# Kernel optimization log

Measured on AMD Instinct MI355X. Metric: run time of the kernel, lower is better.

The kernel has to match this reference:

```python
import jax, jax.numpy as jnp
import numpy as np

C = 512
GROUPS = 32
EPS = 1e-6


def setup_inputs() -> dict:
    key = jax.random.key(0)
    ks = jax.random.split(key, 10)
    B, H, W = 4, 64, 64
    s = 1.0 / np.sqrt(C)
    return {
        "x": jax.random.normal(ks[0], (B, C, H, W), dtype=jnp.float32),
        "gn_weight": jnp.ones((C,), jnp.float32),
        "gn_bias": jnp.zeros((C,), jnp.float32),
        "Wq": jax.random.normal(ks[1], (C, C), jnp.float32) * s,
        "bq": jnp.zeros((C,), jnp.float32),
        "Wk": jax.random.normal(ks[2], (C, C), jnp.float32) * s,
        "bk": jnp.zeros((C,), jnp.float32),
        "Wv": jax.random.normal(ks[3], (C, C), jnp.float32) * s,
        "bv": jnp.zeros((C,), jnp.float32),
        "Wo": jax.random.normal(ks[4], (C, C), jnp.float32) * s,
        "bo": jnp.zeros((C,), jnp.float32),
    }


def _group_norm(x, weight, bias):
    B, Ch, H, W = x.shape
    xg = x.reshape(B, GROUPS, Ch // GROUPS, H, W)
    mean = jnp.mean(xg, axis=(2, 3, 4), keepdims=True)
    var = jnp.var(xg, axis=(2, 3, 4), keepdims=True)
    xg = (xg - mean) * jax.lax.rsqrt(var + EPS)
    h = xg.reshape(B, Ch, H, W)
    return h * weight[None, :, None, None] + bias[None, :, None, None]


def reference(x, gn_weight, gn_bias, Wq, bq, Wk, bk, Wv, bv, Wo, bo):
    B, Ch, H, W = x.shape
    h = _group_norm(x, gn_weight, gn_bias)
    # [B, N, C] with N = H*W spatial tokens
    h = h.reshape(B, Ch, H * W).transpose(0, 2, 1)
    q = h @ Wq.T + bq
    k = h @ Wk.T + bk
    v = h @ Wv.T + bv
    scale = 1.0 / jnp.sqrt(jnp.asarray(Ch, x.dtype))
    scores = jnp.einsum("bnc,bmc->bnm", q, k) * scale  # [B, N, N]
    attn = jax.nn.softmax(scores, axis=-1)
    out = jnp.einsum("bnm,bmc->bnc", attn, v)
    out = out @ Wo.T + bo  # Dropout(0.0) is identity
    out = out.transpose(0, 2, 1).reshape(B, Ch, H, W)
    return x + out
```

## Files before the change

### kernel.cpp

```cpp
#include <hip/hip_runtime.h>
#include <hip/hip_bf16.h>

typedef __attribute__((ext_vector_type(8))) short bf16x8;
typedef __attribute__((ext_vector_type(4))) short bf16x4;
typedef __attribute__((ext_vector_type(4))) float f32x4;

__device__ __forceinline__ short f2bf(float f){
  __hip_bfloat16 h = __float2bfloat16(f);
  return __builtin_bit_cast(short, h);
}
__device__ __forceinline__ float bf2f(short s){
  unsigned u = ((unsigned)(unsigned short)s) << 16;
  return __builtin_bit_cast(float, u);
}

__device__ __forceinline__ void gload_lds16(const short* g, char* l){
  __builtin_amdgcn_global_load_lds(
      (const __attribute__((address_space(1))) void*)g,
      (__attribute__((address_space(3))) void*)l, 16, 0, 0);
}

#define SB0() __builtin_amdgcn_sched_barrier(0)

__global__ __launch_bounds__(256) void gn_stats(const float* __restrict__ x,
// ... 29 lines not shown
                                                short* __restrict__ h){
  __shared__ float tile[128][65];
  int b  = blockIdx.y;
  int n0 = blockIdx.x * 64;
  int t  = threadIdx.x;
  const float* xb = x + (long long)b*512*4096;
  for (int cc = 0; cc < 4; cc++){
    int c0 = cc*128;
    #pragma unroll
    for (int r = 0; r < 128; r += 4){
      int c = r + (t >> 6);
      tile[c][t & 63] = xb[(long long)(c0+c)*4096 + n0 + (t & 63)];
    }
    __syncthreads();
    int n = t >> 2, cp = (t & 3)*32;
    short tmp[32];
    #pragma unroll
    for (int j = 0; j < 32; j++){
      int c = c0 + cp + j;
      float mean = stats[(b*32 + (c >> 4))*2];
      float rstd = stats[(b*32 + (c >> 4))*2 + 1];
      float v = (tile[cp+j][n] - mean)*rstd*gw[c] + gb[c];
      tmp[j] = f2bf(v);
    }
    long long ho = ((long long)b*4096 + n0 + n)*512 + c0 + cp;
    #pragma unroll
    for (int j2 = 0; j2 < 4; j2++){
      bf16x8 v8;
      #pragma unroll
      for (int e = 0; e < 8; e++) v8[e] = tmp[j2*8 + e];
      *(bf16x8*)&h[ho + j2*8] = v8;
    }
    __syncthreads();
  }
}

__global__ __launch_bounds__(256) void f2bf_all(
    const float* __restrict__ w0, const float* __restrict__ w1,
    const float* __restrict__ w2, const float* __restrict__ w3,
    short* __restrict__ o0, short* __restrict__ o1,
    short* __restrict__ o2, short* __restrict__ o3){
  int idx = blockIdx.x*256 + threadIdx.x;
  int m = idx >> 15, r = idx & 32767;
  const float* src = (m==0) ? w0 : (m==1) ? w1 : (m==2) ? w2 : w3;
  short* dst       = (m==0) ? o0 : (m==1) ? o1 : (m==2) ? o2 : o3;
  const float4* p = (const float4*)src + (long long)r*2;
  float4 a = p[0], c = p[1];
  bf16x8 v;
  v[0]=f2bf(a.x); v[1]=f2bf(a.y); v[2]=f2bf(a.z); v[3]=f2bf(a.w);
  v[4]=f2bf(c.x); v[5]=f2bf(c.y); v[6]=f2bf(c.z); v[7]=f2bf(c.w);
  *(bf16x8*)&dst[(long long)r*8] = v;
}

__global__ __launch_bounds__(256) void reduce_den(const float* __restrict__ partial,
                                                  float* __restrict__ inv_den,
                                                  int nrows){
  int r = blockIdx.x*256 + threadIdx.x;
  if (r >= nrows) return;
  const float4* p = (const float4*)(partial + (long long)r*16);
  float4 a = p[0], b = p[1], c = p[2], d = p[3];
  float s = a.x+a.y+a.z+a.w + b.x+b.y+b.z+b.w + c.x+c.y+c.z+c.w + d.x+d.y+d.z+d.w;
  inv_den[r] = 1.f / s;
}

template<int MODE, int BN, int SWZ>
__global__ __launch_bounds__(512, 2) void gemmF(
    const short* __restrict__ A, const short* __restrict__ Bw,
    const float* __restrict__ bias,
    void* __restrict__ outp, const float* __restrict__ resid,
    int M, int Nn, int Kd,
    long long sA, long long sB, long long sO, float scale,
    const float* __restrict__ dptr, float* __restrict__ partial)
{
  constexpr int WARPS_N = BN/64;
  constexpr int WARPS_M = 8/WARPS_N;
  constexpr int WM = 256/WARPS_M;
  constexpr int MF = WM/16;
  constexpr int ABYT = 32768;
  constexpr int BBYT = BN*128;
  constexpr int BUFSZ = ABYT + BBYT;
  constexpr int BH = BBYT/16384;
  constexpr int LOADS = 4 + 2*BH;
  extern __shared__ char smem[];

  int bx, by, bz;
  if constexpr (SWZ == 1){
    int id = blockIdx.x;
    int xcd = id & 7, s = id >> 3;
    int region = xcd + ((s >> 4) << 3);
    int o = s & 15;
    bz = region >> 4;
    bx = (region & 3)*4 + (o & 3);
    by = ((region >> 2) & 3)*4 + (o >> 2);
  } else if constexpr (SWZ == 2){
    int id = blockIdx.x;
    int xcd = id & 7, s = id >> 3;
    int combo = xcd*2 + (s & 1);
    by = combo & 3; bz = combo >> 2;
    bx = s >> 1;
  } else { bx = blockIdx.x; by = blockIdx.y; bz = blockIdx.z; }

  const short* Ab = A + bz*sA;
  const short* Bb = Bw + bz*sB;
  const int m0 = bx*256, n0 = by*BN;
  const int t = threadIdx.x;
  const int lane = t & 63, wid = t >> 6;
  const int g = lane >> 4, lr = lane & 15;
  const int wr = wid / WARPS_N, wc = wid % WARPS_N;
  const long long KdLL = Kd;

  const int r0 = t >> 3, c8 = t & 7;

  auto STAGE_A = [&](int kt, int buf, int h){
    char* d = smem + buf*BUFSZ + h*16384 + t*16;
    #pragma unroll
    for (int j = 0; j < 2; j++){
      int row = h*128 + j*64 + r0;
      gload_lds16(Ab + (long long)(m0+row)*KdLL + (long long)kt*64 + ((c8 ^ (row&7))*8),
                  d + j*8192);
    }
  };
  auto STAGE_B = [&](int kt, int buf, int h){
    char* d = smem + buf*BUFSZ + ABYT + h*16384 + t*16;
    #pragma unroll
    for (int j = 0; j < 2; j++){
      int row = h*128 + j*64 + r0;
      gload_lds16(Bb + (long long)(n0+row)*KdLL + (long long)kt*64 + ((c8 ^ (row&7))*8),
                  d + j*8192);
    }
  };

  int roA[MF], swA[MF], roB[4], swB[4];
  #pragma unroll
  for (int mf = 0; mf < MF; mf++){
    int ra = wr*WM + mf*16 + lr;
    roA[mf] = (ra>>7)*16384 + (ra&127)*128; swA[mf] = ra & 7;
  }
  #pragma unroll
  for (int nf = 0; nf < 4; nf++){
    int rb = wc*64 + nf*16 + lr;
    roB[nf] = ABYT + (rb>>7)*16384 + (rb&127)*128; swB[nf] = rb & 7;
  }

  f32x4 acc[MF][4];
  #pragma unroll
  for (int i = 0; i < MF; i++)
    #pragma unroll
    for (int j = 0; j < 4; j++)
      acc[i][j] = f32x4{0.f,0.f,0.f,0.f};

  const int NT = Kd >> 6;

  STAGE_A(0,0,0); STAGE_A(0,0,1);
  STAGE_B(0,0,0); if constexpr (BH==2) STAGE_B(0,0,1);
  STAGE_A(1,1,0); STAGE_A(1,1,1);
  STAGE_B(1,1,0); if constexpr (BH==2) STAGE_B(1,1,1);
  if constexpr (BH==2) asm volatile("s_waitcnt vmcnt(8)":::"memory");
  else                 asm volatile("s_waitcnt vmcnt(6)":::"memory");
  SB0();
  __builtin_amdgcn_s_barrier();

  for (int kt = 0; kt < NT; ++kt){
    char* base = smem + (kt & 1)*BUFSZ;
    bf16x8 av[MF][2], bv[4][2];
    #pragma unroll
    for (int n = 0; n < 4; n++)
      #pragma unroll
      for (int ks = 0; ks < 2; ks++)
        bv[n][ks] = *(const bf16x8*)(base + roB[n] + (((ks*4+g) ^ swB[n])<<4));
    #pragma unroll
    for (int m = 0; m < MF; m++)
      #pragma unroll
      for (int ks = 0; ks < 2; ks++)
        av[m][ks] = *(const bf16x8*)(base + roA[m] + (((ks*4+g) ^ swA[m])<<4));
    #pragma unroll
    for (int ks = 0; ks < 2; ks++)
      #pragma unroll
      for (int m = 0; m < MF; m++)
        #pragma unroll
        for (int n = 0; n < 4; n++){
          if constexpr (MODE == 1 || MODE == 2)
            acc[m][n] = __builtin_amdgcn_mfma_f32_16x16x32_bf16(av[m][ks], bv[n][ks], acc[m][n], 0,0,0);
          else
            acc[m][n] = __builtin_amdgcn_mfma_f32_16x16x32_bf16(bv[n][ks], av[m][ks], acc[m][n], 0,0,0);
        }
    SB0();
    __builtin_amdgcn_s_barrier();
    SB0();
    if (kt + 2 < NT){
      STAGE_A(kt+2, kt&1, 0); STAGE_A(kt+2, kt&1, 1);
      STAGE_B(kt+2, kt&1, 0); if constexpr (BH==2) STAGE_B(kt+2, kt&1, 1);
      if constexpr (BH==2) asm volatile("s_waitcnt vmcnt(8)":::"memory");
      else                 asm volatile("s_waitcnt vmcnt(6)":::"memory");
    } else {
      asm volatile("s_waitcnt vmcnt(0)":::"memory");
    }
    __builtin_amdgcn_s_barrier();
  }

  if constexpr (MODE == 0){
    short* outb = (short*)outp + bz*sO;
    const bool hb = (bias != nullptr);
    #pragma unroll
    for (int mi = 0; mi < MF; mi++){
      int row = m0 + wr*WM + mi*16 + lr;
      #pragma unroll
      for (int ni = 0; ni < 4; ni++){
        int col = n0 + wc*64 + ni*16 + g*4;
        float b0=0.f,b1=0.f,b2=0.f,b3=0.f;
        if (hb){ float4 bb = *(const float4*)&bias[col]; b0=bb.x; b1=bb.y; b2=bb.z; b3=bb.w; }
        bf16x4 pk;
        pk[0] = f2bf((acc[mi][ni][0] + b0)*scale);
        pk[1] = f2bf((acc[mi][ni][1] + b1)*scale);
        pk[2] = f2bf((acc[mi][ni][2] + b2)*scale);
        pk[3] = f2bf((acc[mi][ni][3] + b3)*scale);
        *(bf16x4*)&outb[(long long)row*Nn + col] = pk;
      }
    }
  } else if constexpr (MODE == 4){
    short* outb = (short*)outp + bz*sO;
    float* rowpart = (float*)smem;
    constexpr float LOG2E = 1.4426950408889634f;
    #pragma unroll
    for (int mi = 0; mi < MF; mi++){
      int lrow = wr*WM + mi*16 + lr;
      int row  = m0 + lrow;
      float rs = 0.f;
      #pragma unroll
      for (int ni = 0; ni < 4; ni++){
        int col = n0 + wc*64 + ni*16 + g*4;
        bf16x4 pk;
        #pragma unroll
        for (int i = 0; i < 4; i++){
          float p = exp2f(acc[mi][ni][i]*LOG2E);
          rs += p;
          pk[i] = f2bf(p);
        }
        *(bf16x4*)&outb[(long long)row*Nn + col] = pk;
      }
      rs += __shfl_xor(rs, 16);
      rs += __shfl_xor(rs, 32);
      if (g == 0) rowpart[lrow*WARPS_N + wc] = rs;
    }
    __syncthreads();
    if (t < 256){
      float s2 = 0.f;
      #pragma unroll
      for (int j = 0; j < WARPS_N; j++) s2 += rowpart[t*WARPS_N + j];
      partial[((long long)bz*4096 + m0 + t)*16 + by] = s2;
    }
  } else if constexpr (MODE == 5){
    short* outb = (short*)outp + bz*sO;
    const float* dd = dptr + (long long)bz*M;
    #pragma unroll
    for (int mi = 0; mi < MF; mi++){
      int row = m0 + wr*WM + mi*16 + lr;
      float inv = dd[row];
      #pragma unroll
      for (int ni = 0; ni < 4; ni++){
        int col = n0 + wc*64 + ni*16 + g*4;
        bf16x4 pk;
        #pragma unroll
        for (int i = 0; i < 4; i++) pk[i] = f2bf(acc[mi][ni][i]*inv);
        *(bf16x4*)&outb[(long long)row*Nn + col] = pk;
      }
    }
  } else if constexpr (MODE == 1){
    short* outb = (short*)outp + bz*sO;
    #pragma unroll
    for (int ni = 0; ni < 4; ni++){
      int col = n0 + wc*64 + ni*16 + lr;
      float bv2 = bias ? bias[col] : 0.f;
      #pragma unroll
      for (int mi = 0; mi < MF; mi++){
        int row = m0 + wr*WM + mi*16 + g*4;
        bf16x4 pk;
        #pragma unroll
        for (int i = 0; i < 4; i++) pk[i] = f2bf((acc[mi][ni][i] + bv2)*scale);
        *(bf16x4*)&outb[(long long)col*M + row] = pk;
      }
    }
  } else {
    float* outb = (float*)outp + bz*sO;
    const float* rx = resid + bz*sO;
    #pragma unroll
    for (int ni = 0; ni < 4; ni++){
      int col = n0 + wc*64 + ni*16 + lr;
      float bv2 = bias[col];
      #pragma unroll
      for (int mi = 0; mi < MF; mi++){
        int row = m0 + wr*WM + mi*16 + g*4;
        long long off = (long long)col*M + row;
        float4 xr = *(const float4*)&rx[off];
        float4 o;
        o.x = acc[mi][ni][0] + bv2 + xr.x;
        o.y = acc[mi][ni][1] + bv2 + xr.y;
        o.z = acc[mi][ni][2] + bv2 + xr.z;
        o.w = acc[mi][ni][3] + bv2 + xr.w;
        *(float4*)&outb[off] = o;
      }
    }
  }
}

extern "C" void kernel_launch(void* const* d_in, const int* in_sizes, int n_in,
                              void* d_out, int out_size, void* d_ws, size_t ws_size,
                              hipStream_t stream)
{
  const float* x   = (const float*)d_in[0];
  const float* gnw = (const float*)d_in[1];
  const float* gnb = (const float*)d_in[2];
  const float* Wq  = (const float*)d_in[3];
  const float* bq  = (const float*)d_in[4];
  const float* Wk  = (const float*)d_in[5];
  const float* bk  = (const float*)d_in[6];
  const float* Wv  = (const float*)d_in[7];
  const float* bvp = (const float*)d_in[8];
  const float* Wo  = (const float*)d_in[9];
  const float* bo  = (const float*)d_in[10];
  float* out = (float*)d_out;

  char* ws = (char*)d_ws;
  const size_t MB = 1ull << 20;
  short* h      = (short*)(ws);
  short* q      = (short*)(ws + 16*MB);
  short* kmat   = (short*)(ws + 32*MB);
  short* vt     = (short*)(ws + 48*MB);
  short* ao     = (short*)(ws + 64*MB);
  short* wqb    = (short*)(ws + 80*MB);
  short* wkb    = wqb + 262144;
  short* wvb    = wkb + 262144;
  short* wob    = wvb + 262144;
  float* stats  = (float*)(ws + 82*MB);
  float* inv_den= (float*)(ws + 82*MB + 8192);
  float* partial= (float*)(ws + 83*MB);
  short* S      = (short*)(ws + 84*MB);

  const int LDS256 = 131072, LDS128 = 98304;
  hipFuncSetAttribute(reinterpret_cast<const void*>(&gemmF<4,256,1>),
                      hipFuncAttributeMaxDynamicSharedMemorySize, LDS256);
  hipFuncSetAttribute(reinterpret_cast<const void*>(&gemmF<4,256,0>),
                      hipFuncAttributeMaxDynamicSharedMemorySize, LDS256);
  hipFuncSetAttribute(reinterpret_cast<const void*>(&gemmF<0,128,0>),
                      hipFuncAttributeMaxDynamicSharedMemorySize, LDS128);
  hipFuncSetAttribute(reinterpret_cast<const void*>(&gemmF<1,128,0>),
                      hipFuncAttributeMaxDynamicSharedMemorySize, LDS128);
  hipFuncSetAttribute(reinterpret_cast<const void*>(&gemmF<2,128,0>),
                      hipFuncAttributeMaxDynamicSharedMemorySize, LDS128);
  hipFuncSetAttribute(reinterpret_cast<const void*>(&gemmF<5,128,2>),
                      hipFuncAttributeMaxDynamicSharedMemorySize, LDS128);
  hipFuncSetAttribute(reinterpret_cast<const void*>(&gemmF<5,128,0>),
                      hipFuncAttributeMaxDynamicSharedMemorySize, LDS128);

  dim3 blk(256);
  dim3 blk512(512);
  gn_stats<<<dim3(128), blk, 0, stream>>>(x, stats);
  gn_apply<<<dim3(64,4), blk, 0, stream>>>(x, stats, gnw, gnb, h);
  f2bf_all<<<dim3(512), blk, 0, stream>>>(Wq, Wk, Wv, Wo, wqb, wkb, wvb, wob);

  const long long sTok = 4096ll*512;
  const long long sS   = 4096ll*4096;
  const float qscale = 0.044194173824159216f;

  gemmF<0,128,0><<<dim3(16,4,4), blk512, LDS128, stream>>>(h, wqb, bq,  q,    nullptr, 4096, 512, 512, sTok, 0, sTok, qscale, nullptr, nullptr);
  gemmF<0,128,0><<<dim3(16,4,4), blk512, LDS128, stream>>>(h, wkb, bk,  kmat, nullptr, 4096, 512, 512, sTok, 0, sTok, 1.f, nullptr, nullptr);
  gemmF<1,128,0><<<dim3(16,4,4), blk512, LDS128, stream>>>(h, wvb, bvp, vt,   nullptr, 4096, 512, 512, sTok, 0, sTok, 1.f, nullptr, nullptr);

  if (ws_size >= 212*MB){
    gemmF<4,256,1><<<dim3(1024), blk512, LDS256, stream>>>(q, kmat, nullptr, S, nullptr, 4096, 4096, 512, sTok, sTok, sS, 1.f, nullptr, partial);
    reduce_den<<<dim3(64), blk, 0, stream>>>(partial, inv_den, 16384);
    gemmF<5,128,2><<<dim3(256), blk512, LDS128, stream>>>(S, vt, nullptr, ao, nullptr, 4096, 512, 4096, sS, sTok, sTok, 1.f, inv_den, nullptr);
  } else {
    for (int b = 0; b < 4; b++){
      gemmF<4,256,0><<<dim3(16,16,1), blk512, LDS256, stream>>>(q + b*sTok, kmat + b*sTok, nullptr, S, nullptr, 4096, 4096, 512, 0, 0, 0, 1.f, nullptr, partial);
      reduce_den<<<dim3(16), blk, 0, stream>>>(partial, inv_den, 4096);
      gemmF<5,128,0><<<dim3(16,4,1), blk512, LDS128, stream>>>(S, vt + b*sTok, nullptr, ao + b*sTok, nullptr, 4096, 512, 4096, 0, 0, 0, 1.f, inv_den, nullptr);
    }
  }

  gemmF<2,128,0><<<dim3(16,4,4), blk512, LDS128, stream>>>(ao, wob, bo, out, x, 4096, 512, 512, sTok, 0, sTok, 1.f, nullptr, nullptr);
}
```

Before: 317.0 us.

## Rework GEMM to 256-thread blocks with K=32 stages and fewer warps

```diff
diff --git a/kernel.cpp b/kernel.cpp
--- a/kernel.cpp
+++ b/kernel.cpp
@@ -117,7 +117,7 @@
 }
 
 template<int MODE, int BN, int SWZ>
-__global__ __launch_bounds__(512, 2) void gemmF(
+__global__ __launch_bounds__(256, 1) void gemmW(
     const short* __restrict__ A, const short* __restrict__ Bw,
     const float* __restrict__ bias,
     void* __restrict__ outp, const float* __restrict__ resid,
@@ -125,15 +125,13 @@
     long long sA, long long sB, long long sO, float scale,
     const float* __restrict__ dptr, float* __restrict__ partial)
 {
-  constexpr int WARPS_N = BN/64;
-  constexpr int WARPS_M = 8/WARPS_N;
-  constexpr int WM = 256/WARPS_M;
-  constexpr int MF = WM/16;
-  constexpr int ABYT = 32768;
-  constexpr int BBYT = BN*128;
+  constexpr int WN = BN/2;
+  constexpr int MF = 8;
+  constexpr int NF = WN/16;
+  constexpr int ABYT = 16384;
+  constexpr int BBYT = BN*64;
   constexpr int BUFSZ = ABYT + BBYT;
-  constexpr int BH = BBYT/16384;
-  constexpr int LOADS = 4 + 2*BH;
+  constexpr int NBG = BN/64;
   extern __shared__ char smem[];
 
   int bx, by, bz;
@@ -159,92 +157,82 @@
   const int t = threadIdx.x;
   const int lane = t & 63, wid = t >> 6;
   const int g = lane >> 4, lr = lane & 15;
-  const int wr = wid / WARPS_N, wc = wid % WARPS_N;
+  const int wr = wid >> 1, wc = wid & 1;
   const long long KdLL = Kd;
 
-  const int r0 = t >> 3, c8 = t & 7;
-
-  auto STAGE_A = [&](int kt, int buf, int h){
-    char* d = smem + buf*BUFSZ + h*16384 + t*16;
-    #pragma unroll
-    for (int j = 0; j < 2; j++){
-      int row = h*128 + j*64 + r0;
-      gload_lds16(Ab + (long long)(m0+row)*KdLL + (long long)kt*64 + ((c8 ^ (row&7))*8),
-                  d + j*8192);
-    }
+  const int srow = t >> 2;
+  const int sch  = (t & 3) ^ ((t >> 3) & 3);
+  const short* pA[4]; const short* pB[NBG];
+  #pragma unroll
+  for (int j = 0; j < 4; j++)
+    pA[j] = Ab + (long long)(m0 + j*64 + srow)*KdLL + sch*8;
+  #pragma unroll
+  for (int j = 0; j < NBG; j++)
+    pB[j] = Bb + (long long)(n0 + j*64 + srow)*KdLL + sch*8;
+  const int t16 = t*16;
+
+  int offA[MF], offB[NF];
+  #pragma unroll
+  for (int mf = 0; mf < MF; mf++){
+    int ra = wr*128 + mf*16 + lr;
+    offA[mf] = ra*64 + ((g ^ ((ra >> 1) & 3)) << 4);
+  }
+  #pragma unroll
+  for (int nf = 0; nf < NF; nf++){
+    int rb = wc*WN + nf*16 + lr;
+    offB[nf] = ABYT + rb*64 + ((g ^ ((rb >> 1) & 3)) << 4);
+  }
+
+  f32x4 acc[MF][NF];
+  #pragma unroll
+  for (int i = 0; i < MF; i++)
+    #pragma unroll
+    for (int j = 0; j < NF; j++)
+      acc[i][j] = f32x4{0.f,0.f,0.f,0.f};
+
+  auto STAGE = [&](int kt, int buf){
+    char* d = smem + buf*BUFSZ;
+    const long long ko = (long long)kt*32;
+    #pragma unroll
+    for (int j = 0; j < 4; j++)
+      gload_lds16(pA[j] + ko, d + j*4096 + t16);
+    #pragma unroll
+    for (int j = 0; j < NBG; j++)
+      gload_lds16(pB[j] + ko, d + ABYT + j*4096 + t16);
   };
-  auto STAGE_B = [&](int kt, int buf, int h){
-    char* d = smem + buf*BUFSZ + ABYT + h*16384 + t*16;
-    #pragma unroll
-    for (int j = 0; j < 2; j++){
-      int row = h*128 + j*64 + r0;
-      gload_lds16(Bb + (long long)(n0+row)*KdLL + (long long)kt*64 + ((c8 ^ (row&7))*8),
-                  d + j*8192);
-    }
-  };
-
-  int roA[MF], swA[MF], roB[4], swB[4];
-  #pragma unroll
-  for (int mf = 0; mf < MF; mf++){
-    int ra = wr*WM + mf*16 + lr;
-    roA[mf] = (ra>>7)*16384 + (ra&127)*128; swA[mf] = ra & 7;
-  }
-  #pragma unroll
-  for (int nf = 0; nf < 4; nf++){
-    int rb = wc*64 + nf*16 + lr;
-    roB[nf] = ABYT + (rb>>7)*16384 + (rb&127)*128; swB[nf] = rb & 7;
-  }
-
-  f32x4 acc[MF][4];
-  #pragma unroll
-  for (int i = 0; i < MF; i++)
-    #pragma unroll
-    for (int j = 0; j < 4; j++)
-      acc[i][j] = f32x4{0.f,0.f,0.f,0.f};
-
-  const int NT = Kd >> 6;
-
-  STAGE_A(0,0,0); STAGE_A(0,0,1);
-  STAGE_B(0,0,0); if constexpr (BH==2) STAGE_B(0,0,1);
-  STAGE_A(1,1,0); STAGE_A(1,1,1);
-  STAGE_B(1,1,0); if constexpr (BH==2) STAGE_B(1,1,1);
-  if constexpr (BH==2) asm volatile("s_waitcnt vmcnt(8)":::"memory");
-  else                 asm volatile("s_waitcnt vmcnt(6)":::"memory");
+
+  const int NT = Kd >> 5;
+
+  STAGE(0, 0);
+  STAGE(1, 1);
+  if constexpr (NBG == 4) asm volatile("s_waitcnt vmcnt(8)":::"memory");
+  else                    asm volatile("s_waitcnt vmcnt(6)":::"memory");
   SB0();
   __builtin_amdgcn_s_barrier();
 
   for (int kt = 0; kt < NT; ++kt){
     char* base = smem + (kt & 1)*BUFSZ;
-    bf16x8 av[MF][2], bv[4][2];
-    #pragma unroll
-    for (int n = 0; n < 4; n++)
-      #pragma unroll
-      for (int ks = 0; ks < 2; ks++)
-        bv[n][ks] = *(const bf16x8*)(base + roB[n] + (((ks*4+g) ^ swB[n])<<4));
+    bf16x8 av[MF], bv[NF];
+    #pragma unroll
+    for (int n = 0; n < NF; n++) bv[n] = *(const bf16x8*)(base + offB[n]);
+    #pragma unroll
+    for (int m = 0; m < MF; m++) av[m] = *(const bf16x8*)(base + offA[m]);
     #pragma unroll
     for (int m = 0; m < MF; m++)
       #pragma unroll
-      for (int ks = 0; ks < 2; ks++)
-        av[m][ks] = *(const bf16x8*)(base + roA[m] + (((ks*4+g) ^ swA[m])<<4));
-    #pragma unroll
-    for (int ks = 0; ks < 2; ks++)
-      #pragma unroll
-      for (int m = 0; m < MF; m++)
-        #pragma unroll
-        for (int n = 0; n < 4; n++){
-          if constexpr (MODE == 1 || MODE == 2)
-            acc[m][n] = __builtin_amdgcn_mfma_f32_16x16x32_bf16(av[m][ks], bv[n][ks], acc[m][n], 0,0,0);
-          else
-            acc[m][n] = __builtin_amdgcn_mfma_f32_16x16x32_bf16(bv[n][ks], av[m][ks], acc[m][n], 0,0,0);
-        }
+      for (int n = 0; n < NF; n++){
+        if constexpr (MODE == 1 || MODE == 2)
+          acc[m][n] = __builtin_amdgcn_mfma_f32_16x16x32_bf16(av[m], bv[n], acc[m][n], 0,0,0);
+        else
+          acc[m][n] = __builtin_amdgcn_mfma_f32_16x16x32_bf16(bv[n], av[m], acc[m][n], 0,0,0);
+      }
     SB0();
     __builtin_amdgcn_s_barrier();
     SB0();
     if (kt + 2 < NT){
-      STAGE_A(kt+2, kt&1, 0); STAGE_A(kt+2, kt&1, 1);
-      STAGE_B(kt+2, kt&1, 0); if constexpr (BH==2) STAGE_B(kt+2, kt&1, 1);
-      if constexpr (BH==2) asm volatile("s_waitcnt vmcnt(8)":::"memory");
-      else                 asm volatile("s_waitcnt vmcnt(6)":::"memory");
+      STAGE(kt + 2, kt & 1);
+      if constexpr (NBG == 4) asm volatile("s_waitcnt vmcnt(8)":::"memory");
+      else                    asm volatile("s_waitcnt vmcnt(6)":::"memory");
     } else {
       asm volatile("s_waitcnt vmcnt(0)":::"memory");
     }
@@ -256,10 +244,10 @@
     const bool hb = (bias != nullptr);
     #pragma unroll
     for (int mi = 0; mi < MF; mi++){
-      int row = m0 + wr*WM + mi*16 + lr;
-      #pragma unroll
-      for (int ni = 0; ni < 4; ni++){
-        int col = n0 + wc*64 + ni*16 + g*4;
+      int row = m0 + wr*128 + mi*16 + lr;
+      #pragma unroll
+      for (int ni = 0; ni < NF; ni++){
+        int col = n0 + wc*WN + ni*16 + g*4;
         float b0=0.f,b1=0.f,b2=0.f,b3=0.f;
         if (hb){ float4 bb = *(const float4*)&bias[col]; b0=bb.x; b1=bb.y; b2=bb.z; b3=bb.w; }
         bf16x4 pk;
@@ -276,12 +264,12 @@
     constexpr float LOG2E = 1.4426950408889634f;
     #pragma unroll
     for (int mi = 0; mi < MF; mi++){
-      int lrow = wr*WM + mi*16 + lr;
+      int lrow = wr*128 + mi*16 + lr;
       int row  = m0 + lrow;
       float rs = 0.f;
       #pragma unroll
-      for (int ni = 0; ni < 4; ni++){
-        int col = n0 + wc*64 + ni*16 + g*4;
+      for (int ni = 0; ni < NF; ni++){
+        int col = n0 + wc*WN + ni*16 + g*4;
         bf16x4 pk;
         #pragma unroll
         for (int i = 0; i < 4; i++){
@@ -293,13 +281,11 @@
       }
       rs += __shfl_xor(rs, 16);
       rs += __shfl_xor(rs, 32);
-      if (g == 0) rowpart[lrow*WARPS_N + wc] = rs;
+      if (g == 0) rowpart[lrow*2 + wc] = rs;
     }
     __syncthreads();
-    if (t < 256){
-      float s2 = 0.f;
-      #pragma unroll
-      for (int j = 0; j < WARPS_N; j++) s2 += rowpart[t*WARPS_N + j];
+    {
+      float s2 = rowpart[t*2] + rowpart[t*2 + 1];
       partial[((long long)bz*4096 + m0 + t)*16 + by] = s2;
     }
   } else if constexpr (MODE == 5){
@@ -307,11 +293,11 @@
     const float* dd = dptr + (long long)bz*M;
     #pragma unroll
     for (int mi = 0; mi < MF; mi++){
-      int row = m0 + wr*WM + mi*16 + lr;
+      int row = m0 + wr*128 + mi*16 + lr;
       float inv = dd[row];
       #pragma unroll
-      for (int ni = 0; ni < 4; ni++){
-        int col = n0 + wc*64 + ni*16 + g*4;
+      for (int ni = 0; ni < NF; ni++){
+        int col = n0 + wc*WN + ni*16 + g*4;
         bf16x4 pk;
         #pragma unroll
         for (int i = 0; i < 4; i++) pk[i] = f2bf(acc[mi][ni][i]*inv);
@@ -321,12 +307,12 @@
   } else if constexpr (MODE == 1){
     short* outb = (short*)outp + bz*sO;
     #pragma unroll
-    for (int ni = 0; ni < 4; ni++){
-      int col = n0 + wc*64 + ni*16 + lr;
+    for (int ni = 0; ni < NF; ni++){
+      int col = n0 + wc*WN + ni*16 + lr;
       float bv2 = bias ? bias[col] : 0.f;
       #pragma unroll
       for (int mi = 0; mi < MF; mi++){
-        int row = m0 + wr*WM + mi*16 + g*4;
+        int row = m0 + wr*128 + mi*16 + g*4;
         bf16x4 pk;
         #pragma unroll
         for (int i = 0; i < 4; i++) pk[i] = f2bf((acc[mi][ni][i] + bv2)*scale);
@@ -337,12 +323,12 @@
     float* outb = (float*)outp + bz*sO;
     const float* rx = resid + bz*sO;
     #pragma unroll
-    for (int ni = 0; ni < 4; ni++){
-      int col = n0 + wc*64 + ni*16 + lr;
+    for (int ni = 0; ni < NF; ni++){
+      int col = n0 + wc*WN + ni*16 + lr;
       float bv2 = bias[col];
       #pragma unroll
       for (int mi = 0; mi < MF; mi++){
-        int row = m0 + wr*WM + mi*16 + g*4;
+        int row = m0 + wr*128 + mi*16 + g*4;
         long long off = (long long)col*M + row;
         float4 xr = *(const float4*)&rx[off];
         float4 o;
@@ -389,24 +375,9 @@
   float* partial= (float*)(ws + 83*MB);
   short* S      = (short*)(ws + 84*MB);
 
-  const int LDS256 = 131072, LDS128 = 98304;
-  hipFuncSetAttribute(reinterpret_cast<const void*>(&gemmF<4,256,1>),
-                      hipFuncAttributeMaxDynamicSharedMemorySize, LDS256);
-  hipFuncSetAttribute(reinterpret_cast<const void*>(&gemmF<4,256,0>),
-                      hipFuncAttributeMaxDynamicSharedMemorySize, LDS256);
-  hipFuncSetAttribute(reinterpret_cast<const void*>(&gemmF<0,128,0>),
-                      hipFuncAttributeMaxDynamicSharedMemorySize, LDS128);
-  hipFuncSetAttribute(reinterpret_cast<const void*>(&gemmF<1,128,0>),
-                      hipFuncAttributeMaxDynamicSharedMemorySize, LDS128);
-  hipFuncSetAttribute(reinterpret_cast<const void*>(&gemmF<2,128,0>),
-                      hipFuncAttributeMaxDynamicSharedMemorySize, LDS128);
-  hipFuncSetAttribute(reinterpret_cast<const void*>(&gemmF<5,128,2>),
-                      hipFuncAttributeMaxDynamicSharedMemorySize, LDS128);
-  hipFuncSetAttribute(reinterpret_cast<const void*>(&gemmF<5,128,0>),
-                      hipFuncAttributeMaxDynamicSharedMemorySize, LDS128);
+  const int SH256 = 65536, SH128 = 49152;
 
   dim3 blk(256);
-  dim3 blk512(512);
   gn_stats<<<dim3(128), blk, 0, stream>>>(x, stats);
   gn_apply<<<dim3(64,4), blk, 0, stream>>>(x, stats, gnw, gnb, h);
   f2bf_all<<<dim3(512), blk, 0, stream>>>(Wq, Wk, Wv, Wo, wqb, wkb, wvb, wob);
@@ -415,21 +386,21 @@
   const long long sS   = 4096ll*4096;
   const float qscale = 0.044194173824159216f;
 
-  gemmF<0,128,0><<<dim3(16,4,4), blk512, LDS128, stream>>>(h, wqb, bq,  q,    nullptr, 4096, 512, 512, sTok, 0, sTok, qscale, nullptr, nullptr);
-  gemmF<0,128,0><<<dim3(16,4,4), blk512, LDS128, stream>>>(h, wkb, bk,  kmat, nullptr, 4096, 512, 512, sTok, 0, sTok, 1.f, nullptr, nullptr);
-  gemmF<1,128,0><<<dim3(16,4,4), blk512, LDS128, stream>>>(h, wvb, bvp, vt,   nullptr, 4096, 512, 512, sTok, 0, sTok, 1.f, nullptr, nullptr);
+  gemmW<0,128,0><<<dim3(16,4,4), blk, SH128, stream>>>(h, wqb, bq,  q,    nullptr, 4096, 512, 512, sTok, 0, sTok, qscale, nullptr, nullptr);
+  gemmW<0,128,0><<<dim3(16,4,4), blk, SH128, stream>>>(h, wkb, bk,  kmat, nullptr, 4096, 512, 512, sTok, 0, sTok, 1.f, nullptr, nullptr);
+  gemmW<1,128,0><<<dim3(16,4,4), blk, SH128, stream>>>(h, wvb, bvp, vt,   nullptr, 4096, 512, 512, sTok, 0, sTok, 1.f, nullptr, nullptr);
 
   if (ws_size >= 212*MB){
-    gemmF<4,256,1><<<dim3(1024), blk512, LDS256, stream>>>(q, kmat, nullptr, S, nullptr, 4096, 4096, 512, sTok, sTok, sS, 1.f, nullptr, partial);
+    gemmW<4,256,1><<<dim3(1024), blk, SH256, stream>>>(q, kmat, nullptr, S, nullptr, 4096, 4096, 512, sTok, sTok, sS, 1.f, nullptr, partial);
     reduce_den<<<dim3(64), blk, 0, stream>>>(partial, inv_den, 16384);
-    gemmF<5,128,2><<<dim3(256), blk512, LDS128, stream>>>(S, vt, nullptr, ao, nullptr, 4096, 512, 4096, sS, sTok, sTok, 1.f, inv_den, nullptr);
+    gemmW<5,128,2><<<dim3(256), blk, SH128, stream>>>(S, vt, nullptr, ao, nullptr, 4096, 512, 4096, sS, sTok, sTok, 1.f, inv_den, nullptr);
   } else {
     for (int b = 0; b < 4; b++){
-      gemmF<4,256,0><<<dim3(16,16,1), blk512, LDS256, stream>>>(q + b*sTok, kmat + b*sTok, nullptr, S, nullptr, 4096, 4096, 512, 0, 0, 0, 1.f, nullptr, partial);
+      gemmW<4,256,0><<<dim3(16,16,1), blk, SH256, stream>>>(q + b*sTok, kmat + b*sTok, nullptr, S, nullptr, 4096, 4096, 512, 0, 0, 0, 1.f, nullptr, partial);
       reduce_den<<<dim3(16), blk, 0, stream>>>(partial, inv_den, 4096);
-      gemmF<5,128,0><<<dim3(16,4,1), blk512, LDS128, stream>>>(S, vt + b*sTok, nullptr, ao + b*sTok, nullptr, 4096, 512, 4096, 0, 0, 0, 1.f, inv_den, nullptr);
-    }
-  }
-
-  gemmF<2,128,0><<<dim3(16,4,4), blk512, LDS128, stream>>>(ao, wob, bo, out, x, 4096, 512, 512, sTok, 0, sTok, 1.f, nullptr, nullptr);
-}
+      gemmW<5,128,0><<<dim3(16,4,1), blk, SH128, stream>>>(S, vt + b*sTok, nullptr, ao + b*sTok, nullptr, 4096, 512, 4096, 0, 0, 0, 1.f, inv_den, nullptr);
+    }
+  }
+
+  gemmW<2,128,0><<<dim3(16,4,4), blk, SH128, stream>>>(ao, wob, bo, out, x, 4096, 512, 512, sTok, 0, sTok, 1.f, nullptr, nullptr);
+}
```

Measured after the change: 396.3 us. 25.0% more time.

## Load GEMM B-operand directly from global into registers, stage only A in LDS

Applied to the files above, without the earlier changes.

```diff
diff --git a/kernel.cpp b/kernel.cpp
--- a/kernel.cpp
+++ b/kernel.cpp
@@ -117,7 +117,7 @@
 }
 
 template<int MODE, int BN, int SWZ>
-__global__ __launch_bounds__(512, 2) void gemmF(
+__global__ __launch_bounds__(512, 2) void gemmG(
     const short* __restrict__ A, const short* __restrict__ Bw,
     const float* __restrict__ bias,
     void* __restrict__ outp, const float* __restrict__ resid,
@@ -126,14 +126,11 @@
     const float* __restrict__ dptr, float* __restrict__ partial)
 {
   constexpr int WARPS_N = BN/64;
-  constexpr int WARPS_M = 8/WARPS_N;
-  constexpr int WM = 256/WARPS_M;
+  constexpr int WM = 256/(8/WARPS_N);
   constexpr int MF = WM/16;
+  constexpr int MH = (MF > 4) ? 2 : 1;
+  constexpr int MFH = MF/MH;
   constexpr int ABYT = 32768;
-  constexpr int BBYT = BN*128;
-  constexpr int BUFSZ = ABYT + BBYT;
-  constexpr int BH = BBYT/16384;
-  constexpr int LOADS = 4 + 2*BH;
   extern __shared__ char smem[];
 
   int bx, by, bz;
@@ -165,7 +162,7 @@
   const int r0 = t >> 3, c8 = t & 7;
 
   auto STAGE_A = [&](int kt, int buf, int h){
-    char* d = smem + buf*BUFSZ + h*16384 + t*16;
+    char* d = smem + buf*ABYT + h*16384 + t*16;
     #pragma unroll
     for (int j = 0; j < 2; j++){
       int row = h*128 + j*64 + r0;
@@ -173,27 +170,24 @@
                   d + j*8192);
     }
   };
-  auto STAGE_B = [&](int kt, int buf, int h){
-    char* d = smem + buf*BUFSZ + ABYT + h*16384 + t*16;
-    #pragma unroll
-    for (int j = 0; j < 2; j++){
-      int row = h*128 + j*64 + r0;
-      gload_lds16(Bb + (long long)(n0+row)*KdLL + (long long)kt*64 + ((c8 ^ (row&7))*8),
-                  d + j*8192);
-    }
-  };
-
-  int roA[MF], swA[MF], roB[4], swB[4];
+
+  int roA[MF], swA[MF];
   #pragma unroll
   for (int mf = 0; mf < MF; mf++){
     int ra = wr*WM + mf*16 + lr;
     roA[mf] = (ra>>7)*16384 + (ra&127)*128; swA[mf] = ra & 7;
   }
-  #pragma unroll
-  for (int nf = 0; nf < 4; nf++){
-    int rb = wc*64 + nf*16 + lr;
-    roB[nf] = ABYT + (rb>>7)*16384 + (rb&127)*128; swB[nf] = rb & 7;
-  }
+
+  const short* pBf = Bb + (long long)(n0 + wc*64 + lr)*KdLL + g*8;
+
+  #define LOAD_BV(DST, KT) do{                                            \
+    _Pragma("unroll")                                                     \
+    for (int _n = 0; _n < 4; _n++)                                        \
+      _Pragma("unroll")                                                   \
+      for (int _ks = 0; _ks < 2; _ks++)                                   \
+        DST[_n][_ks] = *(const bf16x8*)(pBf + (long long)_n*16*KdLL +     \
+                         (long long)(KT)*64 + _ks*32);                    \
+  }while(0)
 
   f32x4 acc[MF][4];
   #pragma unroll
@@ -202,53 +196,51 @@
     for (int j = 0; j < 4; j++)
       acc[i][j] = f32x4{0.f,0.f,0.f,0.f};
 
+  bf16x8 bvA[4][2], bvB[4][2];
   const int NT = Kd >> 6;
 
   STAGE_A(0,0,0); STAGE_A(0,0,1);
-  STAGE_B(0,0,0); if constexpr (BH==2) STAGE_B(0,0,1);
   STAGE_A(1,1,0); STAGE_A(1,1,1);
-  STAGE_B(1,1,0); if constexpr (BH==2) STAGE_B(1,1,1);
-  if constexpr (BH==2) asm volatile("s_waitcnt vmcnt(8)":::"memory");
-  else                 asm volatile("s_waitcnt vmcnt(6)":::"memory");
+  LOAD_BV(bvA, 0);
+  asm volatile("s_waitcnt vmcnt(0)":::"memory");
   SB0();
   __builtin_amdgcn_s_barrier();
 
-  for (int kt = 0; kt < NT; ++kt){
-    char* base = smem + (kt & 1)*BUFSZ;
-    bf16x8 av[MF][2], bv[4][2];
-    #pragma unroll
-    for (int n = 0; n < 4; n++)
-      #pragma unroll
-      for (int ks = 0; ks < 2; ks++)
-        bv[n][ks] = *(const bf16x8*)(base + roB[n] + (((ks*4+g) ^ swB[n])<<4));
-    #pragma unroll
-    for (int m = 0; m < MF; m++)
-      #pragma unroll
-      for (int ks = 0; ks < 2; ks++)
-        av[m][ks] = *(const bf16x8*)(base + roA[m] + (((ks*4+g) ^ swA[m])<<4));
-    #pragma unroll
-    for (int ks = 0; ks < 2; ks++)
-      #pragma unroll
-      for (int m = 0; m < MF; m++)
+  auto BODY = [&](int kt, bf16x8 (&bvC)[4][2], bf16x8 (&bvN)[4][2]){
+    char* base = smem + (kt & 1)*ABYT;
+    if (kt + 1 < NT) LOAD_BV(bvN, kt + 1);
+    #pragma unroll
+    for (int h = 0; h < MH; h++){
+      bf16x8 av[MFH][2];
+      #pragma unroll
+      for (int m = 0; m < MFH; m++)
         #pragma unroll
-        for (int n = 0; n < 4; n++){
-          if constexpr (MODE == 1 || MODE == 2)
-            acc[m][n] = __builtin_amdgcn_mfma_f32_16x16x32_bf16(av[m][ks], bv[n][ks], acc[m][n], 0,0,0);
-          else
-            acc[m][n] = __builtin_amdgcn_mfma_f32_16x16x32_bf16(bv[n][ks], av[m][ks], acc[m][n], 0,0,0);
-        }
+        for (int ks = 0; ks < 2; ks++)
+          av[m][ks] = *(const bf16x8*)(base + roA[h*MFH+m] +
+                        (((ks*4+g) ^ swA[h*MFH+m])<<4));
+      #pragma unroll
+      for (int m = 0; m < MFH; m++)
+        #pragma unroll
+        for (int n = 0; n < 4; n++)
+          #pragma unroll
+          for (int ks = 0; ks < 2; ks++){
+            if constexpr (MODE == 1 || MODE == 2)
+              acc[h*MFH+m][n] = __builtin_amdgcn_mfma_f32_16x16x32_bf16(av[m][ks], bvC[n][ks], acc[h*MFH+m][n], 0,0,0);
+            else
+              acc[h*MFH+m][n] = __builtin_amdgcn_mfma_f32_16x16x32_bf16(bvC[n][ks], av[m][ks], acc[h*MFH+m][n], 0,0,0);
+          }
+    }
     SB0();
     __builtin_amdgcn_s_barrier();
     SB0();
-    if (kt + 2 < NT){
-      STAGE_A(kt+2, kt&1, 0); STAGE_A(kt+2, kt&1, 1);
-      STAGE_B(kt+2, kt&1, 0); if constexpr (BH==2) STAGE_B(kt+2, kt&1, 1);
-      if constexpr (BH==2) asm volatile("s_waitcnt vmcnt(8)":::"memory");
-      else                 asm volatile("s_waitcnt vmcnt(6)":::"memory");
-    } else {
-      asm volatile("s_waitcnt vmcnt(0)":::"memory");
-    }
+    if (kt + 2 < NT){ STAGE_A(kt+2, kt&1, 0); STAGE_A(kt+2, kt&1, 1); }
+    asm volatile("s_waitcnt vmcnt(0)":::"memory");
     __builtin_amdgcn_s_barrier();
+  };
+
+  for (int kt = 0; kt < NT; kt += 2){
+    BODY(kt,     bvA, bvB);
+    BODY(kt + 1, bvB, bvA);
   }
 
   if constexpr (MODE == 0){
@@ -354,6 +346,7 @@
       }
     }
   }
+  #undef LOAD_BV
 }
 
 extern "C" void kernel_launch(void* const* d_in, const int* in_sizes, int n_in,
@@ -389,21 +382,7 @@
   float* partial= (float*)(ws + 83*MB);
   short* S      = (short*)(ws + 84*MB);
 
-  const int LDS256 = 131072, LDS128 = 98304;
-  hipFuncSetAttribute(reinterpret_cast<const void*>(&gemmF<4,256,1>),
-                      hipFuncAttributeMaxDynamicSharedMemorySize, LDS256);
-  hipFuncSetAttribute(reinterpret_cast<const void*>(&gemmF<4,256,0>),
-                      hipFuncAttributeMaxDynamicSharedMemorySize, LDS256);
-  hipFuncSetAttribute(reinterpret_cast<const void*>(&gemmF<0,128,0>),
-                      hipFuncAttributeMaxDynamicSharedMemorySize, LDS128);
-  hipFuncSetAttribute(reinterpret_cast<const void*>(&gemmF<1,128,0>),
-                      hipFuncAttributeMaxDynamicSharedMemorySize, LDS128);
-  hipFuncSetAttribute(reinterpret_cast<const void*>(&gemmF<2,128,0>),
-                      hipFuncAttributeMaxDynamicSharedMemorySize, LDS128);
-  hipFuncSetAttribute(reinterpret_cast<const void*>(&gemmF<5,128,2>),
-                      hipFuncAttributeMaxDynamicSharedMemorySize, LDS128);
-  hipFuncSetAttribute(reinterpret_cast<const void*>(&gemmF<5,128,0>),
-                      hipFuncAttributeMaxDynamicSharedMemorySize, LDS128);
+  const int SH = 65536;
 
   dim3 blk(256);
   dim3 blk512(512);
@@ -415,21 +394,21 @@
   const long long sS   = 4096ll*4096;
   const float qscale = 0.044194173824159216f;
 
-  gemmF<0,128,0><<<dim3(16,4,4), blk512, LDS128, stream>>>(h, wqb, bq,  q,    nullptr, 4096, 512, 512, sTok, 0, sTok, qscale, nullptr, nullptr);
-  gemmF<0,128,0><<<dim3(16,4,4), blk512, LDS128, stream>>>(h, wkb, bk,  kmat, nullptr, 4096, 512, 512, sTok, 0, sTok, 1.f, nullptr, nullptr);
-  gemmF<1,128,0><<<dim3(16,4,4), blk512, LDS128, stream>>>(h, wvb, bvp, vt,   nullptr, 4096, 512, 512, sTok, 0, sTok, 1.f, nullptr, nullptr);
+  gemmG<0,128,0><<<dim3(16,4,4), blk512, SH, stream>>>(h, wqb, bq,  q,    nullptr, 4096, 512, 512, sTok, 0, sTok, qscale, nullptr, nullptr);
+  gemmG<0,128,0><<<dim3(16,4,4), blk512, SH, stream>>>(h, wkb, bk,  kmat, nullptr, 4096, 512, 512, sTok, 0, sTok, 1.f, nullptr, nullptr);
+  gemmG<1,128,0><<<dim3(16,4,4), blk512, SH, stream>>>(h, wvb, bvp, vt,   nullptr, 4096, 512, 512, sTok, 0, sTok, 1.f, nullptr, nullptr);
 
   if (ws_size >= 212*MB){
-    gemmF<4,256,1><<<dim3(1024), blk512, LDS256, stream>>>(q, kmat, nullptr, S, nullptr, 4096, 4096, 512, sTok, sTok, sS, 1.f, nullptr, partial);
+    gemmG<4,256,1><<<dim3(1024), blk512, SH, stream>>>(q, kmat, nullptr, S, nullptr, 4096, 4096, 512, sTok, sTok, sS, 1.f, nullptr, partial);
     reduce_den<<<dim3(64), blk, 0, stream>>>(partial, inv_den, 16384);
-    gemmF<5,128,2><<<dim3(256), blk512, LDS128, stream>>>(S, vt, nullptr, ao, nullptr, 4096, 512, 4096, sS, sTok, sTok, 1.f, inv_den, nullptr);
+    gemmG<5,128,2><<<dim3(256), blk512, SH, stream>>>(S, vt, nullptr, ao, nullptr, 4096, 512, 4096, sS, sTok, sTok, 1.f, inv_den, nullptr);
   } else {
     for (int b = 0; b < 4; b++){
-      gemmF<4,256,0><<<dim3(16,16,1), blk512, LDS256, stream>>>(q + b*sTok, kmat + b*sTok, nullptr, S, nullptr, 4096, 4096, 512, 0, 0, 0, 1.f, nullptr, partial);
+      gemmG<4,256,0><<<dim3(16,16,1), blk512, SH, stream>>>(q + b*sTok, kmat + b*sTok, nullptr, S, nullptr, 4096, 4096, 512, 0, 0, 0, 1.f, nullptr, partial);
       reduce_den<<<dim3(16), blk, 0, stream>>>(partial, inv_den, 4096);
-      gemmF<5,128,0><<<dim3(16,4,1), blk512, LDS128, stream>>>(S, vt + b*sTok, nullptr, ao + b*sTok, nullptr, 4096, 512, 4096, 0, 0, 0, 1.f, inv_den, nullptr);
-    }
-  }
-
-  gemmF<2,128,0><<<dim3(16,4,4), blk512, LDS128, stream>>>(ao, wob, bo, out, x, 4096, 512, 512, sTok, 0, sTok, 1.f, nullptr, nullptr);
-}
+      gemmG<5,128,0><<<dim3(16,4,1), blk512, SH, stream>>>(S, vt + b*sTok, nullptr, ao + b*sTok, nullptr, 4096, 512, 4096, 0, 0, 0, 1.f, inv_den, nullptr);
+    }
+  }
+
+  gemmG<2,128,0><<<dim3(16,4,4), blk512, SH, stream>>>(ao, wob, bo, out, x, 4096, 512, 512, sTok, 0, sTok, 1.f, nullptr, nullptr);
+}
```

Result: slower. 498.6 us (+57.3%).

## Fuse QKV projections into one GEMM and use smaller 128x128 tiles for PV/out

Applied to the files above, without the earlier changes.

```diff
diff --git a/kernel.cpp b/kernel.cpp
--- a/kernel.cpp
+++ b/kernel.cpp
@@ -105,6 +105,14 @@
   *(bf16x8*)&dst[(long long)r*8] = v;
 }
 
+__global__ __launch_bounds__(256) void bcat(const float* __restrict__ bq,
+                                            const float* __restrict__ bk,
+                                            const float* __restrict__ bv,
+                                            float* __restrict__ o){
+  int t = blockIdx.x*256 + threadIdx.x;
+  if (t < 512){ o[t] = bq[t]; o[512+t] = bk[t]; o[1024+t] = bv[t]; }
+}
+
 __global__ __launch_bounds__(256) void reduce_den(const float* __restrict__ partial,
                                                   float* __restrict__ inv_den,
                                                   int nrows){
@@ -116,8 +124,8 @@
   inv_den[r] = 1.f / s;
 }
 
-template<int MODE, int BN, int SWZ>
-__global__ __launch_bounds__(512, 2) void gemmF(
+template<int MODE, int TM, int BN, int TH, int SWZ>
+__global__ __launch_bounds__(TH, 2) void gemmF(
     const short* __restrict__ A, const short* __restrict__ Bw,
     const float* __restrict__ bias,
     void* __restrict__ outp, const float* __restrict__ resid,
@@ -125,15 +133,16 @@
     long long sA, long long sB, long long sO, float scale,
     const float* __restrict__ dptr, float* __restrict__ partial)
 {
+  constexpr int WAVES   = TH/64;
   constexpr int WARPS_N = BN/64;
-  constexpr int WARPS_M = 8/WARPS_N;
-  constexpr int WM = 256/WARPS_M;
+  constexpr int WARPS_M = WAVES/WARPS_N;
+  constexpr int WM = TM/WARPS_M;
   constexpr int MF = WM/16;
-  constexpr int ABYT = 32768;
-  constexpr int BBYT = BN*128;
-  constexpr int BUFSZ = ABYT + BBYT;
-  constexpr int BH = BBYT/16384;
-  constexpr int LOADS = 4 + 2*BH;
+  constexpr int ABYT = TM*128;
+  constexpr int BUFSZ = (TM+BN)*128;
+  constexpr int APASS = (TM*128)/(TH*16);
+  constexpr int BPASS = (BN*128)/(TH*16);
+  constexpr int LOADS = APASS + BPASS;
   extern __shared__ char smem[];
 
   int bx, by, bz;
@@ -155,31 +164,28 @@
 
   const short* Ab = A + bz*sA;
   const short* Bb = Bw + bz*sB;
-  const int m0 = bx*256, n0 = by*BN;
+  const int m0 = bx*TM, n0 = by*BN;
   const int t = threadIdx.x;
   const int lane = t & 63, wid = t >> 6;
   const int g = lane >> 4, lr = lane & 15;
   const int wr = wid / WARPS_N, wc = wid % WARPS_N;
   const long long KdLL = Kd;
 
-  const int r0 = t >> 3, c8 = t & 7;
-
-  auto STAGE_A = [&](int kt, int buf, int h){
-    char* d = smem + buf*BUFSZ + h*16384 + t*16;
-    #pragma unroll
-    for (int j = 0; j < 2; j++){
-      int row = h*128 + j*64 + r0;
-      gload_lds16(Ab + (long long)(m0+row)*KdLL + (long long)kt*64 + ((c8 ^ (row&7))*8),
-                  d + j*8192);
-    }
-  };
-  auto STAGE_B = [&](int kt, int buf, int h){
-    char* d = smem + buf*BUFSZ + ABYT + h*16384 + t*16;
-    #pragma unroll
-    for (int j = 0; j < 2; j++){
-      int row = h*128 + j*64 + r0;
-      gload_lds16(Bb + (long long)(n0+row)*KdLL + (long long)kt*64 + ((c8 ^ (row&7))*8),
-                  d + j*8192);
+  auto STAGE = [&](int kt, int buf){
+    char* d0 = smem + buf*BUFSZ;
+    #pragma unroll
+    for (int p = 0; p < APASS; p++){
+      int f = p*TH*16 + t*16;
+      int row = f >> 7, ch = (f >> 4) & 7;
+      gload_lds16(Ab + (long long)(m0+row)*KdLL + (long long)kt*64 + ((ch ^ (row&7))*8),
+                  d0 + f);
+    }
+    #pragma unroll
+    for (int p = 0; p < BPASS; p++){
+      int f = p*TH*16 + t*16;
+      int row = f >> 7, ch = (f >> 4) & 7;
+      gload_lds16(Bb + (long long)(n0+row)*KdLL + (long long)kt*64 + ((ch ^ (row&7))*8),
+                  d0 + ABYT + f);
     }
   };
 
@@ -187,12 +193,12 @@
   #pragma unroll
   for (int mf = 0; mf < MF; mf++){
     int ra = wr*WM + mf*16 + lr;
-    roA[mf] = (ra>>7)*16384 + (ra&127)*128; swA[mf] = ra & 7;
+    roA[mf] = ra*128; swA[mf] = ra & 7;
   }
   #pragma unroll
   for (int nf = 0; nf < 4; nf++){
     int rb = wc*64 + nf*16 + lr;
-    roB[nf] = ABYT + (rb>>7)*16384 + (rb&127)*128; swB[nf] = rb & 7;
+    roB[nf] = ABYT + rb*128; swB[nf] = rb & 7;
   }
 
   f32x4 acc[MF][4];
@@ -204,12 +210,10 @@
 
   const int NT = Kd >> 6;
 
-  STAGE_A(0,0,0); STAGE_A(0,0,1);
-  STAGE_B(0,0,0); if constexpr (BH==2) STAGE_B(0,0,1);
-  STAGE_A(1,1,0); STAGE_A(1,1,1);
-  STAGE_B(1,1,0); if constexpr (BH==2) STAGE_B(1,1,1);
-  if constexpr (BH==2) asm volatile("s_waitcnt vmcnt(8)":::"memory");
-  else                 asm volatile("s_waitcnt vmcnt(6)":::"memory");
+  STAGE(0, 0);
+  STAGE(1, 1);
+  if constexpr (LOADS == 8) asm volatile("s_waitcnt vmcnt(8)":::"memory");
+  else                      asm volatile("s_waitcnt vmcnt(6)":::"memory");
   SB0();
   __builtin_amdgcn_s_barrier();
 
@@ -232,7 +236,7 @@
       for (int m = 0; m < MF; m++)
         #pragma unroll
         for (int n = 0; n < 4; n++){
-          if constexpr (MODE == 1 || MODE == 2)
+          if constexpr (MODE == 2)
             acc[m][n] = __builtin_amdgcn_mfma_f32_16x16x32_bf16(av[m][ks], bv[n][ks], acc[m][n], 0,0,0);
           else
             acc[m][n] = __builtin_amdgcn_mfma_f32_16x16x32_bf16(bv[n][ks], av[m][ks], acc[m][n], 0,0,0);
@@ -241,36 +245,16 @@
     __builtin_amdgcn_s_barrier();
     SB0();
     if (kt + 2 < NT){
-      STAGE_A(kt+2, kt&1, 0); STAGE_A(kt+2, kt&1, 1);
-      STAGE_B(kt+2, kt&1, 0); if constexpr (BH==2) STAGE_B(kt+2, kt&1, 1);
-      if constexpr (BH==2) asm volatile("s_waitcnt vmcnt(8)":::"memory");
-      else                 asm volatile("s_waitcnt vmcnt(6)":::"memory");
+      STAGE(kt + 2, kt & 1);
+      if constexpr (LOADS == 8) asm volatile("s_waitcnt vmcnt(8)":::"memory");
+      else                      asm volatile("s_waitcnt vmcnt(6)":::"memory");
     } else {
       asm volatile("s_waitcnt vmcnt(0)":::"memory");
     }
     __builtin_amdgcn_s_barrier();
   }
 
-  if constexpr (MODE == 0){
-    short* outb = (short*)outp + bz*sO;
-    const bool hb = (bias != nullptr);
-    #pragma unroll
-    for (int mi = 0; mi < MF; mi++){
-      int row = m0 + wr*WM + mi*16 + lr;
-      #pragma unroll
-      for (int ni = 0; ni < 4; ni++){
-        int col = n0 + wc*64 + ni*16 + g*4;
-        float b0=0.f,b1=0.f,b2=0.f,b3=0.f;
-        if (hb){ float4 bb = *(const float4*)&bias[col]; b0=bb.x; b1=bb.y; b2=bb.z; b3=bb.w; }
-        bf16x4 pk;
-        pk[0] = f2bf((acc[mi][ni][0] + b0)*scale);
-        pk[1] = f2bf((acc[mi][ni][1] + b1)*scale);
-        pk[2] = f2bf((acc[mi][ni][2] + b2)*scale);
-        pk[3] = f2bf((acc[mi][ni][3] + b3)*scale);
-        *(bf16x4*)&outb[(long long)row*Nn + col] = pk;
-      }
-    }
-  } else if constexpr (MODE == 4){
+  if constexpr (MODE == 4){
     short* outb = (short*)outp + bz*sO;
     float* rowpart = (float*)smem;
     constexpr float LOG2E = 1.4426950408889634f;
@@ -296,7 +280,7 @@
       if (g == 0) rowpart[lrow*WARPS_N + wc] = rs;
     }
     __syncthreads();
-    if (t < 256){
+    if (t < TM){
       float s2 = 0.f;
       #pragma unroll
       for (int j = 0; j < WARPS_N; j++) s2 += rowpart[t*WARPS_N + j];
@@ -318,19 +302,33 @@
         *(bf16x4*)&outb[(long long)row*Nn + col] = pk;
       }
     }
-  } else if constexpr (MODE == 1){
-    short* outb = (short*)outp + bz*sO;
-    #pragma unroll
-    for (int ni = 0; ni < 4; ni++){
-      int col = n0 + wc*64 + ni*16 + lr;
-      float bv2 = bias ? bias[col] : 0.f;
-      #pragma unroll
-      for (int mi = 0; mi < MF; mi++){
-        int row = m0 + wr*WM + mi*16 + g*4;
+  } else if constexpr (MODE == 6){
+    const int seg = by >> 2;
+    const long long base = (long long)bz*sO;
+    short* qp  = (short*)outp;
+    short* kp  = (short*)partial;
+    short* vtp = (short*)dptr;
+    #pragma unroll
+    for (int mi = 0; mi < MF; mi++){
+      int row = m0 + wr*WM + mi*16 + lr;
+      #pragma unroll
+      for (int ni = 0; ni < 4; ni++){
+        int col = n0 + wc*64 + ni*16 + g*4;
+        float4 bb = *(const float4*)&bias[col];
+        int cq = col - seg*512;
+        float sc = (seg == 0) ? scale : 1.f;
         bf16x4 pk;
-        #pragma unroll
-        for (int i = 0; i < 4; i++) pk[i] = f2bf((acc[mi][ni][i] + bv2)*scale);
-        *(bf16x4*)&outb[(long long)col*M + row] = pk;
+        pk[0] = f2bf((acc[mi][ni][0] + bb.x)*sc);
+        pk[1] = f2bf((acc[mi][ni][1] + bb.y)*sc);
+        pk[2] = f2bf((acc[mi][ni][2] + bb.z)*sc);
+        pk[3] = f2bf((acc[mi][ni][3] + bb.w)*sc);
+        if (seg == 0)      *(bf16x4*)&qp[base + (long long)row*512 + cq] = pk;
+        else if (seg == 1) *(bf16x4*)&kp[base + (long long)row*512 + cq] = pk;
+        else {
+          #pragma unroll
+          for (int i = 0; i < 4; i++)
+            vtp[base + (long long)(cq+i)*4096 + row] = pk[i];
+        }
       }
     }
   } else {
@@ -380,56 +378,61 @@
   short* kmat   = (short*)(ws + 32*MB);
   short* vt     = (short*)(ws + 48*MB);
   short* ao     = (short*)(ws + 64*MB);
-  short* wqb    = (short*)(ws + 80*MB);
-  short* wkb    = wqb + 262144;
-  short* wvb    = wkb + 262144;
-  short* wob    = wvb + 262144;
+  short* wqkv   = (short*)(ws + 80*MB);
+  short* wob    = wqkv + 3*262144;
   float* stats  = (float*)(ws + 82*MB);
   float* inv_den= (float*)(ws + 82*MB + 8192);
+  float* bqkv   = (float*)(ws + 82*MB + 131072);
   float* partial= (float*)(ws + 83*MB);
   short* S      = (short*)(ws + 84*MB);
 
-  const int LDS256 = 131072, LDS128 = 98304;
-  hipFuncSetAttribute(reinterpret_cast<const void*>(&gemmF<4,256,1>),
-                      hipFuncAttributeMaxDynamicSharedMemorySize, LDS256);
-  hipFuncSetAttribute(reinterpret_cast<const void*>(&gemmF<4,256,0>),
-                      hipFuncAttributeMaxDynamicSharedMemorySize, LDS256);
-  hipFuncSetAttribute(reinterpret_cast<const void*>(&gemmF<0,128,0>),
-                      hipFuncAttributeMaxDynamicSharedMemorySize, LDS128);
-  hipFuncSetAttribute(reinterpret_cast<const void*>(&gemmF<1,128,0>),
-                      hipFuncAttributeMaxDynamicSharedMemorySize, LDS128);
-  hipFuncSetAttribute(reinterpret_cast<const void*>(&gemmF<2,128,0>),
-                      hipFuncAttributeMaxDynamicSharedMemorySize, LDS128);
-  hipFuncSetAttribute(reinterpret_cast<const void*>(&gemmF<5,128,2>),
-                      hipFuncAttributeMaxDynamicSharedMemorySize, LDS128);
-  hipFuncSetAttribute(reinterpret_cast<const void*>(&gemmF<5,128,0>),
-                      hipFuncAttributeMaxDynamicSharedMemorySize, LDS128);
+  const int LDS_SC = 131072;
+  const int LDS_QK = 98304;
+  const int LDS_PV = 65536;
+  hipFuncSetAttribute(reinterpret_cast<const void*>(&gemmF<4,256,256,512,1>),
+                      hipFuncAttributeMaxDynamicSharedMemorySize, LDS_SC);
+  hipFuncSetAttribute(reinterpret_cast<const void*>(&gemmF<4,256,256,512,0>),
+                      hipFuncAttributeMaxDynamicSharedMemorySize, LDS_SC);
+  hipFuncSetAttribute(reinterpret_cast<const void*>(&gemmF<6,256,128,512,0>),
+                      hipFuncAttributeMaxDynamicSharedMemorySize, LDS_QK);
+  hipFuncSetAttribute(reinterpret_cast<const void*>(&gemmF<5,128,128,256,2>),
+                      hipFuncAttributeMaxDynamicSharedMemorySize, LDS_PV);
+  hipFuncSetAttribute(reinterpret_cast<const void*>(&gemmF<5,128,128,256,0>),
+                      hipFuncAttributeMaxDynamicSharedMemorySize, LDS_PV);
+  hipFuncSetAttribute(reinterpret_cast<const void*>(&gemmF<2,128,128,256,0>),
+                      hipFuncAttributeMaxDynamicSharedMemorySize, LDS_PV);
 
   dim3 blk(256);
   dim3 blk512(512);
   gn_stats<<<dim3(128), blk, 0, stream>>>(x, stats);
   gn_apply<<<dim3(64,4), blk, 0, stream>>>(x, stats, gnw, gnb, h);
-  f2bf_all<<<dim3(512), blk, 0, stream>>>(Wq, Wk, Wv, Wo, wqb, wkb, wvb, wob);
+  f2bf_all<<<dim3(512), blk, 0, stream>>>(Wq, Wk, Wv, Wo, wqkv, wqkv + 262144, wqkv + 2*262144, wob);
+  bcat<<<dim3(2), blk, 0, stream>>>(bq, bk, bvp, bqkv);
 
   const long long sTok = 4096ll*512;
   const long long sS   = 4096ll*4096;
   const float qscale = 0.044194173824159216f;
 
-  gemmF<0,128,0><<<dim3(16,4,4), blk512, LDS128, stream>>>(h, wqb, bq,  q,    nullptr, 4096, 512, 512, sTok, 0, sTok, qscale, nullptr, nullptr);
-  gemmF<0,128,0><<<dim3(16,4,4), blk512, LDS128, stream>>>(h, wkb, bk,  kmat, nullptr, 4096, 512, 512, sTok, 0, sTok, 1.f, nullptr, nullptr);
-  gemmF<1,128,0><<<dim3(16,4,4), blk512, LDS128, stream>>>(h, wvb, bvp, vt,   nullptr, 4096, 512, 512, sTok, 0, sTok, 1.f, nullptr, nullptr);
+  gemmF<6,256,128,512,0><<<dim3(16,12,4), blk512, LDS_QK, stream>>>(
+      h, wqkv, bqkv, q, nullptr, 4096, 1536, 512, sTok, 0, sTok, qscale,
+      (const float*)vt, (float*)kmat);
 
   if (ws_size >= 212*MB){
-    gemmF<4,256,1><<<dim3(1024), blk512, LDS256, stream>>>(q, kmat, nullptr, S, nullptr, 4096, 4096, 512, sTok, sTok, sS, 1.f, nullptr, partial);
+    gemmF<4,256,256,512,1><<<dim3(1024), blk512, LDS_SC, stream>>>(
+        q, kmat, nullptr, S, nullptr, 4096, 4096, 512, sTok, sTok, sS, 1.f, nullptr, partial);
     reduce_den<<<dim3(64), blk, 0, stream>>>(partial, inv_den, 16384);
-    gemmF<5,128,2><<<dim3(256), blk512, LDS128, stream>>>(S, vt, nullptr, ao, nullptr, 4096, 512, 4096, sS, sTok, sTok, 1.f, inv_den, nullptr);
+    gemmF<5,128,128,256,2><<<dim3(512), blk, LDS_PV, stream>>>(
+        S, vt, nullptr, ao, nullptr, 4096, 512, 4096, sS, sTok, sTok, 1.f, inv_den, nullptr);
   } else {
     for (int b = 0; b < 4; b++){
-      gemmF<4,256,0><<<dim3(16,16,1), blk512, LDS256, stream>>>(q + b*sTok, kmat + b*sTok, nullptr, S, nullptr, 4096, 4096, 512, 0, 0, 0, 1.f, nullptr, partial);
+      gemmF<4,256,256,512,0><<<dim3(16,16,1), blk512, LDS_SC, stream>>>(
+          q + b*sTok, kmat + b*sTok, nullptr, S, nullptr, 4096, 4096, 512, 0, 0, 0, 1.f, nullptr, partial);
       reduce_den<<<dim3(16), blk, 0, stream>>>(partial, inv_den, 4096);
-      gemmF<5,128,0><<<dim3(16,4,1), blk512, LDS128, stream>>>(S, vt + b*sTok, nullptr, ao + b*sTok, nullptr, 4096, 512, 4096, 0, 0, 0, 1.f, inv_den, nullptr);
-    }
-  }
-
-  gemmF<2,128,0><<<dim3(16,4,4), blk512, LDS128, stream>>>(ao, wob, bo, out, x, 4096, 512, 512, sTok, 0, sTok, 1.f, nullptr, nullptr);
-}
+      gemmF<5,128,128,256,0><<<dim3(32,4,1), blk, LDS_PV, stream>>>(
+          S, vt + b*sTok, nullptr, ao + b*sTok, nullptr, 4096, 512, 4096, 0, 0, 0, 1.f, inv_den, nullptr);
+    }
+  }
+
+  gemmF<2,128,128,256,0><<<dim3(32,4,4), blk, LDS_PV, stream>>>(
+      ao, wob, bo, out, x, 4096, 512, 512, sTok, 0, sTok, 1.f, nullptr, nullptr);
+}
```

Result: faster. 298.7 us (-5.8%).
